# Performance work log

Measured on AMD Instinct MI355X. Metric: run time of the kernel, lower is better.

## Reference

```python
import jax, jax.numpy as jnp
import numpy as np
import math

B_SZ, T, D_IN, D_OUT, N = 8, 4096, 1024, 1024, 512
RMIN, RMAX, MAX_PHASE = 0.9, 1.0, 6.283


def setup_inputs() -> dict:
    key = jax.random.key(0)
    ks = jax.random.split(key, 9)
    x = jax.random.normal(ks[0], (B_SZ, T, D_IN), dtype=jnp.float32)
    u1 = jax.random.uniform(ks[1], (N,), dtype=jnp.float32)
    u2 = jax.random.uniform(ks[2], (N,), dtype=jnp.float32)
    nu_log = jnp.log(-0.5 * jnp.log(u1 * (RMAX + RMIN) * (RMAX - RMIN) + RMIN ** 2))
    theta_log = jnp.log(MAX_PHASE * u2)
    lam_mod = jnp.exp(-jnp.exp(nu_log))
    gamma_log = jnp.log(jnp.sqrt(1.0 - jnp.square(lam_mod)))
    B_re = jax.random.normal(ks[3], (N, D_IN), dtype=jnp.float32) / math.sqrt(2 * D_IN)
    B_im = jax.random.normal(ks[4], (N, D_IN), dtype=jnp.float32) / math.sqrt(2 * D_IN)
    C_re = jax.random.normal(ks[5], (D_OUT, N), dtype=jnp.float32) / math.sqrt(N)
    C_im = jax.random.normal(ks[6], (D_OUT, N), dtype=jnp.float32) / math.sqrt(N)
    D = jax.random.normal(ks[7], (D_OUT, D_IN), dtype=jnp.float32) / math.sqrt(D_IN)
    return {"x": x, "nu_log": nu_log, "theta_log": theta_log, "gamma_log": gamma_log,
            "B_re": B_re, "B_im": B_im, "C_re": C_re, "C_im": C_im, "D": D}


def reference(x, nu_log, theta_log, gamma_log, B_re, B_im, C_re, C_im, D):
    # Diagonal complex transition Lambda = exp(-exp(nu_log)) * exp(i*exp(theta_log))
    lam = jnp.exp(-jnp.exp(nu_log) + 1j * jnp.exp(theta_log))  # [N] complex64
    gamma = jnp.exp(gamma_log)  # [N]
    Bmat = B_re + 1j * B_im  # [N, D_IN]
    # Input projection for all timesteps at once: b_t = gamma * (B @ u_t)
    Bu = jnp.einsum('bti,ni->btn', x.astype(Bmat.dtype), Bmat) * gamma  # [B,T,N] complex
    # Parallel (associative) scan of x_t = lam * x_{t-1} + b_t over the time axis
    A = jnp.broadcast_to(lam, Bu.shape)

    def combine(e1, e2):
        a1, b1 = e1
        a2, b2 = e2
        return a1 * a2, a2 * b1 + b2

    _, states = jax.lax.associative_scan(combine, (A, Bu), axis=1)  # states: [B,T,N] complex
    Cmat = C_re + 1j * C_im  # [D_OUT, N]
    y = jnp.einsum('btn,on->bto', states, Cmat).real + jnp.einsum('bti,oi->bto', x, D)
    return y
```

## Files before the change

kernel.cpp:

```cpp
#include <hip/hip_runtime.h>
#include <stdint.h>


#define BSZ   8
#define TLEN  4096
#define DIN   1024
#define DOUT  1024
#define NST   512
#define M_TOT (BSZ * TLEN)
#define NC    32
#define CL    128
#define PLA   4096
#define BUFS  12288

typedef __attribute__((ext_vector_type(8))) short bf16x8;
typedef __attribute__((ext_vector_type(4))) float f32x4;

__device__ __forceinline__ float s2f(short s) {
  unsigned v = ((unsigned)(unsigned short)s) << 16;
  return __builtin_bit_cast(float, v);
}
__device__ __forceinline__ short f2s_rne(float f) {
  unsigned u = __builtin_bit_cast(unsigned, f);
  unsigned r = (u + 0x7FFFu + ((u >> 16) & 1u)) >> 16;
  return (short)r;
}
__device__ __forceinline__ void round8(const float4 v0, const float4 v1, bf16x8& hv) {
  const float f[8] = {v0.x, v0.y, v0.z, v0.w, v1.x, v1.y, v1.z, v1.w};
  #pragma unroll
  for (int j = 0; j < 8; ++j) hv[j] = f2s_rne(f[j]);
}

__device__ __forceinline__ void gload16(const short* g, short* l) {
  __builtin_amdgcn_global_load_lds(
      (const __attribute__((address_space(1))) void*)g,
      (__attribute__((address_space(3))) void*)l, 16, 0, 0);
}


__device__ __forceinline__ void stage_cx(
    const short* __restrict__ Ag, const short* __restrict__ Wg,
    const int lda, const int ldb, const int m0, const int n0, const int k0,
    short* lbuf, const int w, const int lane)
{
  const int q  = (lane & 3) ^ ((lane >> 3) & 3);
  const int gr = lane >> 2;
  #pragma unroll
  for (int j = 0; j < 3; ++j) {
    const int ch = w * 3 + j;
    const short* g;
    int r0, ld, dst;
    if (ch < 8) { g = Ag; r0 = m0 + ch * 16;        ld = lda; dst = ch * 512; }
    else        { g = Wg; r0 = n0 + (ch - 8) * 16;  ld = ldb; dst = PLA + (ch - 8) * 512; }
    gload16(g + (size_t)(r0 + gr) * ld + k0 + q * 8, lbuf + dst);
  }
}

template<int NT>
__device__ __forceinline__ void gemm_pl(
    const short* __restrict__ Ap, const short* __restrict__ Wp,
    const int lda, const int ldb, const int m0, const int n0, const int tid,
    f32x4 (&acc)[4][4], short* lds)
{
  const int lane = tid & 63, w = tid >> 6, wm = w >> 2, wn = w & 3;
  const int lr = lane & 15, kg = lane >> 4;
  const int qo = (kg ^ ((lr >> 1) & 3)) * 8;

  stage_cx(Ap, Wp, lda, ldb, m0, n0, 0, lds, w, lane);

  for (int k = 0; k < NT; ++k) {
    short* cur = lds + (k & 1) * BUFS;
    if (k + 1 < NT) {
      stage_cx(Ap, Wp, lda, ldb, m0, n0, (k + 1) * 32,
               lds + ((k + 1) & 1) * BUFS, w, lane);
      asm volatile("s_waitcnt vmcnt(3)" ::: "memory");
    } else {
      asm volatile("s_waitcnt vmcnt(0)" ::: "memory");
    }
    __builtin_amdgcn_s_barrier();

    bf16x8 bw[4];
    #pragma unroll
    for (int ph = 0; ph < 2; ++ph) {
      if (ph == 0) {
        #pragma unroll
        for (int ni = 0; ni < 4; ++ni)
          bw[ni] = *(const bf16x8*)&cur[PLA + (wn * 64 + ni * 16 + lr) * 32 + qo];
      }
      const int mi0 = ph * 2;
      const bf16x8 a0 = *(const bf16x8*)&cur[(wm * 64 + mi0 * 16 + lr) * 32 + qo];
      const bf16x8 a1 = *(const bf16x8*)&cur[(wm * 64 + (mi0 + 1) * 16 + lr) * 32 + qo];
      __builtin_amdgcn_s_barrier();
      asm volatile("s_waitcnt lgkmcnt(0)" ::: "memory");
      __builtin_amdgcn_sched_barrier(0);
      __builtin_amdgcn_s_setprio(1);
      #pragma unroll
      for (int ni = 0; ni < 4; ++ni) {
        acc[mi0][ni]     = __builtin_amdgcn_mfma_f32_16x16x32_bf16(a0, bw[ni], acc[mi0][ni], 0, 0, 0);
        acc[mi0 + 1][ni] = __builtin_amdgcn_mfma_f32_16x16x32_bf16(a1, bw[ni], acc[mi0 + 1][ni], 0, 0, 0);
      }
      __builtin_amdgcn_s_setprio(0);
      __builtin_amdgcn_s_barrier();
    }
  }
}

__device__ __forceinline__ void gemm_fb(
    const float* __restrict__ Af, const short* __restrict__ Wp,
    const int lda, const int ldb, const int K, const int m0, const int n0, const int tid,
    f32x4 (&acc)[4][4], short* lds)
{
  const int lane = tid & 63, w = tid >> 6, wm = w >> 2, wn = w & 3;
  const int r = tid & 127, e = (tid >> 7) & 3;
  float4 pa[2];
  {
    const float* p = Af + (size_t)(m0 + r) * lda + e * 8;
    pa[0] = *(const float4*)(p);
    pa[1] = *(const float4*)(p + 4);
  }
  for (int k0 = 0; k0 < K; k0 += 32) {
    __syncthreads();
    {
      bf16x8 hv;
      round8(pa[0], pa[1], hv);
      const int f = (r >> 1) & 3;
      *(bf16x8*)&lds[r * 32 + ((e ^ f) * 8)] = hv;
    }
    {
      const int q = (lane & 3) ^ ((lane >> 3) & 3);
      const int gr = lane >> 2;
      #pragma unroll
      for (int i = 0; i < 2; ++i)
        gload16(Wp + (size_t)(n0 + (2 * w + i) * 16 + gr) * ldb + k0 + q * 8,
                lds + PLA + (2 * w + i) * 512);
    }
    __syncthreads();
    if (k0 + 32 < K) {
      const float* p = Af + (size_t)(m0 + r) * lda + (k0 + 32) + e * 8;
      pa[0] = *(const float4*)(p);
      pa[1] = *(const float4*)(p + 4);
    }
    const int lr = lane & 15, kg = lane >> 4;
    const int qo = (kg ^ ((lr >> 1) & 3)) * 8;
    bf16x8 aw[4], bw[4];
    #pragma unroll
    for (int mi = 0; mi < 4; ++mi)
      aw[mi] = *(const bf16x8*)&lds[(wm * 64 + mi * 16 + lr) * 32 + qo];
    #pragma unroll
    for (int ni = 0; ni < 4; ++ni)
      bw[ni] = *(const bf16x8*)&lds[PLA + (wn * 64 + ni * 16 + lr) * 32 + qo];
    #pragma unroll
    for (int ni = 0; ni < 4; ++ni)
      #pragma unroll
      for (int mi = 0; mi < 4; ++mi)
        acc[mi][ni] = __builtin_amdgcn_mfma_f32_16x16x32_bf16(aw[mi], bw[ni], acc[mi][ni], 0, 0, 0);
  }
  __syncthreads();
}

__device__ __forceinline__ void map_mn4(const int bid, int& mb, int& nb) {
  const int xcd = bid & 7;
  const int j   = bid >> 3;
  mb = xcd * 32 + (j >> 2);
  nb = j & 3;
}

__global__ __launch_bounds__(256) void wround_k(const float* __restrict__ src,
    short* __restrict__ h, const int n4, const float sgn)
{
  const int i = blockIdx.x * 256 + threadIdx.x;
  if (i >= n4) return;
  const float4 v = ((const float4*)src)[i];
  short4 hv;
  hv.x = f2s_rne(sgn * v.x); hv.y = f2s_rne(sgn * v.y);
  hv.z = f2s_rne(sgn * v.z); hv.w = f2s_rne(sgn * v.w);
  ((short4*)h)[i] = hv;
}

template<bool XAG>
__global__ __launch_bounds__(512, 4) void bu_mfma(
    const float* __restrict__ x, const short* __restrict__ xw,
    const short* __restrict__ Brw, const short* __restrict__ Biw,
    const float* __restrict__ gamma,
    short* __restrict__ bu_re, short* __restrict__ bu_im)
{
  __shared__ short lds[2 * BUFS];
  f32x4 acc[4][4] = {};
  const int tid = threadIdx.x;
  int mb, nbk;
  map_mn4(blockIdx.x, mb, nbk);
  const int m0  = mb * 128;
  const int n0s = nbk * 256;
  const bool re = (n0s < NST);
  const int nb0 = n0s & (NST - 1);
  const short* Bw = re ? Brw : Biw;

  if constexpr (XAG)
    gemm_pl<32>(xw, Bw, DIN, DIN, m0, nb0, tid, acc, lds);
  else
    gemm_fb(x, Bw, DIN, DIN, DIN, m0, nb0, tid, acc, lds);

  short* Hp = re ? bu_re : bu_im;
  const int lane = tid & 63, w = tid >> 6, wm = w >> 2, wn = w & 3;
  const int lr = lane & 15, lq = lane >> 4;
  #pragma unroll
  for (int ni = 0; ni < 4; ++ni) {
    const int nb = nb0 + wn * 64 + ni * 16 + lr;
    const float g = gamma[nb];
    #pragma unroll
    for (int mi = 0; mi < 4; ++mi)
      #pragma unroll
      for (int j = 0; j < 4; ++j) {
        const size_t m = (size_t)m0 + wm * 64 + mi * 16 + lq * 4 + j;
        Hp[m * NST + nb] = f2s_rne(acc[mi][ni][j] * g);
      }
  }
}

__global__ void params_k(const float* __restrict__ nulog, const float* __restrict__ thlog,
                         const float* __restrict__ glog,
                         float2* __restrict__ lam, float2* __restrict__ lamL,
                         float* __restrict__ gamma)
{
  const int n = blockIdx.x * 256 + threadIdx.x;
  if (n >= NST) return;
  const float nu = expf(nulog[n]);
  const float th = expf(thlog[n]);
  const float mod = expf(-nu);
  float s, c;
  sincosf(th, &s, &c);
  lam[n] = make_float2(mod * c, mod * s);
  const float modL = expf(-(float)CL * nu);
  float sL, cL;
  sincosf((float)CL * th, &sL, &cL);
  lamL[n] = make_float2(modL * cL, modL * sL);
  gamma[n] = expf(glog[n]);
}

__global__ __launch_bounds__(256) void scan_partial(
    const short* __restrict__ bu_re, const short* __restrict__ bu_im,
    const float2* __restrict__ lam, float2* __restrict__ carry)
{
  const int g = blockIdx.x * 256 + threadIdx.x;
  const int n2 = g & 255;
  const int c  = (g >> 8) & (NC - 1);
  const int b  = g >> 13;
  const int n  = n2 * 2;
  const float2 L0 = lam[n], L1 = lam[n + 1];
  const short2* R = (const short2*)bu_re;
  const short2* I = (const short2*)bu_im;
  size_t idx = ((size_t)b * TLEN + (size_t)c * CL) * (NST / 2) + n2;
  float sr0 = 0.f, si0 = 0.f, sr1 = 0.f, si1 = 0.f;
  #pragma unroll 4
  for (int t = 0; t < CL; ++t, idx += NST / 2) {
    const short2 vr = R[idx], vi = I[idx];
    const float br0 = s2f(vr.x), br1 = s2f(vr.y);
    const float bi0 = s2f(vi.x), bi1 = s2f(vi.y);
    float nr = fmaf(L0.x, sr0, fmaf(-L0.y, si0, br0));
    float ni = fmaf(L0.x, si0, fmaf( L0.y, sr0, bi0));
    sr0 = nr; si0 = ni;
    nr = fmaf(L1.x, sr1, fmaf(-L1.y, si1, br1));
    ni = fmaf(L1.x, si1, fmaf( L1.y, sr1, bi1));
    sr1 = nr; si1 = ni;
  }
  const size_t cb = (size_t)(b * NC + c) * NST + n;
  carry[cb]     = make_float2(sr0, si0);
  carry[cb + 1] = make_float2(sr1, si1);
}

__global__ __launch_bounds__(256) void scan_carry(
    float2* __restrict__ carry, const float2* __restrict__ lamL)
{
  const int g = blockIdx.x * 256 + threadIdx.x;
  const int n = g & (NST - 1);
  const int b = g >> 9;
  const float2 P = lamL[n];
  float sr = 0.f, si = 0.f;
  for (int c = 0; c < NC; ++c) {
    const size_t idx = (size_t)(b * NC + c) * NST + n;
    const float2 v = carry[idx];
    carry[idx] = make_float2(sr, si);
    const float nr = fmaf(P.x, sr, fmaf(-P.y, si, v.x));
    const float ni = fmaf(P.x, si, fmaf( P.y, sr, v.y));
    sr = nr; si = ni;
  }
}

__global__ __launch_bounds__(256) void scan_final(
    short* __restrict__ bu_re, short* __restrict__ bu_im,
    const float2* __restrict__ lam, const float2* __restrict__ carry)
{
  const int g = blockIdx.x * 256 + threadIdx.x;
  const int n2 = g & 255;
  const int c  = (g >> 8) & (NC - 1);
  const int b  = g >> 13;
  const int n  = n2 * 2;
  const float2 L0 = lam[n], L1 = lam[n + 1];
  const size_t cb = (size_t)(b * NC + c) * NST + n;
  const float2 ci0 = carry[cb], ci1 = carry[cb + 1];
  short2* R = (short2*)bu_re;
  short2* I = (short2*)bu_im;
  size_t idx = ((size_t)b * TLEN + (size_t)c * CL) * (NST / 2) + n2;
  float sr0 = ci0.x, si0 = ci0.y, sr1 = ci1.x, si1 = ci1.y;
  #pragma unroll 4
  for (int t = 0; t < CL; ++t, idx += NST / 2) {
    const short2 vr = R[idx], vi = I[idx];
    const float br0 = s2f(vr.x), br1 = s2f(vr.y);
    const float bi0 = s2f(vi.x), bi1 = s2f(vi.y);
    float nr = fmaf(L0.x, sr0, fmaf(-L0.y, si0, br0));
    float ni = fmaf(L0.x, si0, fmaf( L0.y, sr0, bi0));
    sr0 = nr; si0 = ni;
    nr = fmaf(L1.x, sr1, fmaf(-L1.y, si1, br1));
    ni = fmaf(L1.x, si1, fmaf( L1.y, sr1, bi1));
    sr1 = nr; si1 = ni;
    short2 so;
    so.x = f2s_rne(sr0); so.y = f2s_rne(sr1);
    R[idx] = so;
    so.x = f2s_rne(si0); so.y = f2s_rne(si1);
    I[idx] = so;
  }
}

template<bool XAG>
__global__ __launch_bounds__(512, 4) void out_mfma(
    const short* __restrict__ st_re, const short* __restrict__ st_im,
    const float* __restrict__ x, const short* __restrict__ xw,
    const short* __restrict__ Crw, const short* __restrict__ Ciw,
    const short* __restrict__ Dw,
    float* __restrict__ y)
{
  __shared__ short lds[2 * BUFS];
  f32x4 acc[4][4] = {};
  const int tid = threadIdx.x;
  int mb, nbk;
  map_mn4(blockIdx.x, mb, nbk);
  const int m0 = mb * 128;
  const int o0 = nbk * 256;

  gemm_pl<16>(st_re, Crw, NST, NST, m0, o0, tid, acc, lds);
  gemm_pl<16>(st_im, Ciw, NST, NST, m0, o0, tid, acc, lds);
  if constexpr (XAG)
    gemm_pl<32>(xw, Dw, DIN, DIN, m0, o0, tid, acc, lds);
  else
    gemm_fb(x, Dw, DIN, DIN, DIN, m0, o0, tid, acc, lds);

  const int lane = tid & 63, w = tid >> 6, wm = w >> 2, wn = w & 3;
  const int lr = lane & 15, lq = lane >> 4;
  #pragma unroll
  for (int mi = 0; mi < 4; ++mi)
    #pragma unroll
    for (int j = 0; j < 4; ++j) {
      const size_t m = (size_t)m0 + wm * 64 + mi * 16 + lq * 4 + j;
      #pragma unroll
      for (int ni = 0; ni < 4; ++ni)
        y[m * DOUT + o0 + wn * 64 + ni * 16 + lr] = acc[mi][ni][j];
    }
}

extern "C" void kernel_launch(void* const* d_in, const int* in_sizes, int n_in,
                              void* d_out, int out_size, void* d_ws, size_t ws_size,
                              hipStream_t stream)
{
  (void)in_sizes; (void)n_in; (void)out_size;
  const float* x     = (const float*)d_in[0];
  const float* nulog = (const float*)d_in[1];
  const float* thlog = (const float*)d_in[2];
  const float* glog  = (const float*)d_in[3];
  const float* Bre   = (const float*)d_in[4];
  const float* Bim   = (const float*)d_in[5];
  const float* Cre   = (const float*)d_in[6];
  const float* Cim   = (const float*)d_in[7];
  const float* Dm    = (const float*)d_in[8];
  float* y = (float*)d_out;

  const size_t PLANE  = (size_t)M_TOT * NST;
  const size_t XPLANE = (size_t)M_TOT * DIN;
  short*  bu_re = (short*)d_ws;
  short*  bu_im = bu_re + PLANE;
  float2* carry = (float2*)(bu_im + PLANE);
  float2* lam   = carry + (size_t)BSZ * NC * NST;
  float2* lamL  = lam + NST;
  float*  gamma = (float*)(lamL + NST);

  char* wp = (char*)(gamma + NST);
  wp = (char*)(((uintptr_t)wp + 255) & ~(uintptr_t)255);
  short* Brw = (short*)wp;
  short* Biw = Brw + (size_t)NST * DIN;
  short* Crw = Biw + (size_t)NST * DIN;
  short* Ciw = Crw + (size_t)DOUT * NST;
  short* Dw  = Ciw + (size_t)DOUT * NST;
  short* xw  = Dw  + (size_t)DOUT * DIN;
  const size_t needed_full = (size_t)((char*)(xw + XPLANE) - (char*)d_ws);
  const bool full = (ws_size >= needed_full);

  params_k<<<2, 256, 0, stream>>>(nulog, thlog, glog, lam, lamL, gamma);

  const int nB4 = (NST * DIN) / 4, nC4 = (DOUT * NST) / 4, nD4 = (DOUT * DIN) / 4;
  wround_k<<<(nB4 + 255) / 256, 256, 0, stream>>>(Bre, Brw, nB4,  1.0f);
  wround_k<<<(nB4 + 255) / 256, 256, 0, stream>>>(Bim, Biw, nB4,  1.0f);
  wround_k<<<(nC4 + 255) / 256, 256, 0, stream>>>(Cre, Crw, nC4,  1.0f);
  wround_k<<<(nC4 + 255) / 256, 256, 0, stream>>>(Cim, Ciw, nC4, -1.0f);
  wround_k<<<(nD4 + 255) / 256, 256, 0, stream>>>(Dm,  Dw,  nD4,  1.0f);

  if (full) {
    const int nX4 = (int)(XPLANE / 4);
    wround_k<<<(nX4 + 255) / 256, 256, 0, stream>>>(x, xw, nX4, 1.0f);
    bu_mfma<true><<<1024, 512, 0, stream>>>(x, xw, Brw, Biw, gamma, bu_re, bu_im);
  } else {
    bu_mfma<false><<<1024, 512, 0, stream>>>(x, xw, Brw, Biw, gamma, bu_re, bu_im);
  }

  scan_partial<<<(BSZ * NC * (NST / 2)) / 256, 256, 0, stream>>>(bu_re, bu_im, lam, carry);
  scan_carry<<<(BSZ * NST) / 256, 256, 0, stream>>>(carry, lamL);
  scan_final<<<(BSZ * NC * (NST / 2)) / 256, 256, 0, stream>>>(bu_re, bu_im, lam, carry);

  if (full) {
    out_mfma<true><<<1024, 512, 0, stream>>>(bu_re, bu_im, x, xw, Crw, Ciw, Dw, y);
  } else {
    out_mfma<false><<<1024, 512, 0, stream>>>(bu_re, bu_im, x, xw, Crw, Ciw, Dw, y);
  }
}
```

Before: 314.8 us.

## Enlarge GEMM block tile to 256x256 for projection and output kernels

Adds a 256x256 block-tile GEMM path (each wave computes 128x64 with 8x4 MFMA fragments) and uses it for the Bu projection and the output projection when the workspace allows a bf16 copy of x. Grids shrink from 1024 to 512 blocks. The larger tile halves global and LDS traffic per FLOP and amortizes barriers, at the cost of higher register pressure, 64KB LDS per block and occupancy capped at 2 blocks per CU. The fallback paths are kept as separate kernels.

```diff
diff --git a/kernel.cpp b/kernel.cpp
--- a/kernel.cpp
+++ b/kernel.cpp
@@ -10,8 +10,12 @@
 #define M_TOT (BSZ * TLEN)
 #define NC    32
 #define CL    128
+
+#define WOFF  8192
+#define NBUF  16384
+
 #define PLA   4096
-#define BUFS  12288
+#define OBUFS 12288
 
 typedef __attribute__((ext_vector_type(8))) short bf16x8;
 typedef __attribute__((ext_vector_type(4))) float f32x4;
@@ -37,6 +41,82 @@
       (__attribute__((address_space(3))) void*)l, 16, 0, 0);
 }
 
+
+__device__ __forceinline__ void stage256(
+    const short* __restrict__ Ag, const short* __restrict__ Wg,
+    const int lda, const int ldb, const int m0, const int n0, const int k0,
+    short* lbuf, const int w, const int lane)
+{
+  const int q  = (lane & 3) ^ ((lane >> 3) & 3);
+  const int gr = lane >> 2;
+  #pragma unroll
+  for (int j = 0; j < 4; ++j) {
+    const int ch = w * 4 + j;
+    const short* g;
+    int r0, ld, dst;
+    if (ch < 16) { g = Ag; r0 = m0 + ch * 16;        ld = lda; dst = ch * 512; }
+    else         { g = Wg; r0 = n0 + (ch - 16) * 16; ld = ldb; dst = WOFF + (ch - 16) * 512; }
+    gload16(g + (size_t)(r0 + gr) * ld + k0 + q * 8, lbuf + dst);
+  }
+}
+
+template<int NT>
+__device__ __forceinline__ void gemm256(
+    const short* __restrict__ Ap, const short* __restrict__ Wp,
+    const int lda, const int ldb, const int m0, const int n0, const int tid,
+    f32x4 (&acc)[8][4], short* lds)
+{
+  const int lane = tid & 63, w = tid >> 6, wm = w >> 2, wn = w & 3;
+  const int lr = lane & 15, kg = lane >> 4;
+  const int qo = (kg ^ ((lr >> 1) & 3)) * 8;
+
+  stage256(Ap, Wp, lda, ldb, m0, n0, 0, lds, w, lane);
+
+  for (int k = 0; k < NT; ++k) {
+    short* cur = lds + (k & 1) * NBUF;
+    if (k + 1 < NT) {
+      stage256(Ap, Wp, lda, ldb, m0, n0, (k + 1) * 32,
+               lds + ((k + 1) & 1) * NBUF, w, lane);
+      asm volatile("s_waitcnt vmcnt(4)" ::: "memory");
+    } else {
+      asm volatile("s_waitcnt vmcnt(0)" ::: "memory");
+    }
+    __builtin_amdgcn_s_barrier();
+
+    bf16x8 wv[4];
+    #pragma unroll
+    for (int ph = 0; ph < 2; ++ph) {
+      if (ph == 0) {
+        #pragma unroll
+        for (int nf = 0; nf < 4; ++nf)
+          wv[nf] = *(const bf16x8*)&cur[WOFF + (wn * 64 + nf * 16 + lr) * 32 + qo];
+      }
+      bf16x8 af[4];
+      #pragma unroll
+      for (int mi = 0; mi < 4; ++mi)
+        af[mi] = *(const bf16x8*)&cur[(wm * 128 + (ph * 4 + mi) * 16 + lr) * 32 + qo];
+      __builtin_amdgcn_s_barrier();
+      asm volatile("s_waitcnt lgkmcnt(0)" ::: "memory");
+      __builtin_amdgcn_sched_barrier(0);
+      __builtin_amdgcn_s_setprio(1);
+      #pragma unroll
+      for (int nf = 0; nf < 4; ++nf)
+        #pragma unroll
+        for (int mi = 0; mi < 4; ++mi)
+          acc[ph * 4 + mi][nf] =
+              __builtin_amdgcn_mfma_f32_16x16x32_bf16(af[mi], wv[nf], acc[ph * 4 + mi][nf], 0, 0, 0);
+      __builtin_amdgcn_s_setprio(0);
+      __builtin_amdgcn_s_barrier();
+    }
+  }
+}
+
+__device__ __forceinline__ void map256(const int bid, int& mb, int& nb) {
+  const int xcd = bid & 7;
+  const int j   = bid >> 3;
+  mb = xcd * 16 + (j >> 2);
+  nb = j & 3;
+}
 
 __device__ __forceinline__ void stage_cx(
     const short* __restrict__ Ag, const short* __restrict__ Wg,
@@ -56,6 +136,59 @@
   }
 }
 
+__device__ __forceinline__ void gemm_fb(
+    const float* __restrict__ Af, const short* __restrict__ Wp,
+    const int lda, const int ldb, const int K, const int m0, const int n0, const int tid,
+    f32x4 (&acc)[4][4], short* lds)
+{
+  const int lane = tid & 63, w = tid >> 6, wm = w >> 2, wn = w & 3;
+  const int r = tid & 127, e = (tid >> 7) & 3;
+  float4 pa[2];
+  {
+    const float* p = Af + (size_t)(m0 + r) * lda + e * 8;
+    pa[0] = *(const float4*)(p);
+    pa[1] = *(const float4*)(p + 4);
+  }
+  for (int k0 = 0; k0 < K; k0 += 32) {
+    __syncthreads();
+    {
+      bf16x8 hv;
+      round8(pa[0], pa[1], hv);
+      const int f = (r >> 1) & 3;
+      *(bf16x8*)&lds[r * 32 + ((e ^ f) * 8)] = hv;
+    }
+    {
+      const int q = (lane & 3) ^ ((lane >> 3) & 3);
+      const int gr = lane >> 2;
+      #pragma unroll
+      for (int i = 0; i < 2; ++i)
+        gload16(Wp + (size_t)(n0 + (2 * w + i) * 16 + gr) * ldb + k0 + q * 8,
+                lds + PLA + (2 * w + i) * 512);
+    }
+    __syncthreads();
+    if (k0 + 32 < K) {
+      const float* p = Af + (size_t)(m0 + r) * lda + (k0 + 32) + e * 8;
+      pa[0] = *(const float4*)(p);
+      pa[1] = *(const float4*)(p + 4);
+    }
+    const int lr = lane & 15, kg = lane >> 4;
+    const int qo = (kg ^ ((lr >> 1) & 3)) * 8;
+    bf16x8 aw[4], bw[4];
+    #pragma unroll
+    for (int mi = 0; mi < 4; ++mi)
+      aw[mi] = *(const bf16x8*)&lds[(wm * 64 + mi * 16 + lr) * 32 + qo];
+    #pragma unroll
+    for (int ni = 0; ni < 4; ++ni)
+      bw[ni] = *(const bf16x8*)&lds[PLA + (wn * 64 + ni * 16 + lr) * 32 + qo];
+    #pragma unroll
+    for (int ni = 0; ni < 4; ++ni)
+      #pragma unroll
+      for (int mi = 0; mi < 4; ++mi)
+        acc[mi][ni] = __builtin_amdgcn_mfma_f32_16x16x32_bf16(aw[mi], bw[ni], acc[mi][ni], 0, 0, 0);
+  }
+  __syncthreads();
+}
+
 template<int NT>
 __device__ __forceinline__ void gemm_pl(
     const short* __restrict__ Ap, const short* __restrict__ Wp,
@@ -65,20 +198,16 @@
   const int lane = tid & 63, w = tid >> 6, wm = w >> 2, wn = w & 3;
   const int lr = lane & 15, kg = lane >> 4;
   const int qo = (kg ^ ((lr >> 1) & 3)) * 8;
-
   stage_cx(Ap, Wp, lda, ldb, m0, n0, 0, lds, w, lane);
-
   for (int k = 0; k < NT; ++k) {
-    short* cur = lds + (k & 1) * BUFS;
+    short* cur = lds + (k & 1) * OBUFS;
     if (k + 1 < NT) {
-      stage_cx(Ap, Wp, lda, ldb, m0, n0, (k + 1) * 32,
-               lds + ((k + 1) & 1) * BUFS, w, lane);
+      stage_cx(Ap, Wp, lda, ldb, m0, n0, (k + 1) * 32, lds + ((k + 1) & 1) * OBUFS, w, lane);
       asm volatile("s_waitcnt vmcnt(3)" ::: "memory");
     } else {
       asm volatile("s_waitcnt vmcnt(0)" ::: "memory");
     }
     __builtin_amdgcn_s_barrier();
-
     bf16x8 bw[4];
     #pragma unroll
     for (int ph = 0; ph < 2; ++ph) {
@@ -105,59 +234,6 @@
   }
 }
 
-__device__ __forceinline__ void gemm_fb(
-    const float* __restrict__ Af, const short* __restrict__ Wp,
-    const int lda, const int ldb, const int K, const int m0, const int n0, const int tid,
-    f32x4 (&acc)[4][4], short* lds)
-{
-  const int lane = tid & 63, w = tid >> 6, wm = w >> 2, wn = w & 3;
-  const int r = tid & 127, e = (tid >> 7) & 3;
-  float4 pa[2];
-  {
-    const float* p = Af + (size_t)(m0 + r) * lda + e * 8;
-    pa[0] = *(const float4*)(p);
-    pa[1] = *(const float4*)(p + 4);
-  }
-  for (int k0 = 0; k0 < K; k0 += 32) {
-    __syncthreads();
-    {
-      bf16x8 hv;
-      round8(pa[0], pa[1], hv);
-      const int f = (r >> 1) & 3;
-      *(bf16x8*)&lds[r * 32 + ((e ^ f) * 8)] = hv;
-    }
-    {
-      const int q = (lane & 3) ^ ((lane >> 3) & 3);
-      const int gr = lane >> 2;
-      #pragma unroll
-      for (int i = 0; i < 2; ++i)
-        gload16(Wp + (size_t)(n0 + (2 * w + i) * 16 + gr) * ldb + k0 + q * 8,
-                lds + PLA + (2 * w + i) * 512);
-    }
-    __syncthreads();
-    if (k0 + 32 < K) {
-      const float* p = Af + (size_t)(m0 + r) * lda + (k0 + 32) + e * 8;
-      pa[0] = *(const float4*)(p);
-      pa[1] = *(const float4*)(p + 4);
-    }
-    const int lr = lane & 15, kg = lane >> 4;
-    const int qo = (kg ^ ((lr >> 1) & 3)) * 8;
-    bf16x8 aw[4], bw[4];
-    #pragma unroll
-    for (int mi = 0; mi < 4; ++mi)
-      aw[mi] = *(const bf16x8*)&lds[(wm * 64 + mi * 16 + lr) * 32 + qo];
-    #pragma unroll
-    for (int ni = 0; ni < 4; ++ni)
-      bw[ni] = *(const bf16x8*)&lds[PLA + (wn * 64 + ni * 16 + lr) * 32 + qo];
-    #pragma unroll
-    for (int ni = 0; ni < 4; ++ni)
-      #pragma unroll
-      for (int mi = 0; mi < 4; ++mi)
-        acc[mi][ni] = __builtin_amdgcn_mfma_f32_16x16x32_bf16(aw[mi], bw[ni], acc[mi][ni], 0, 0, 0);
-  }
-  __syncthreads();
-}
-
 __device__ __forceinline__ void map_mn4(const int bid, int& mb, int& nb) {
   const int xcd = bid & 7;
   const int j   = bid >> 3;
@@ -177,14 +253,48 @@
   ((short4*)h)[i] = hv;
 }
 
-template<bool XAG>
-__global__ __launch_bounds__(512, 4) void bu_mfma(
-    const float* __restrict__ x, const short* __restrict__ xw,
+__global__ __launch_bounds__(512, 2) void bu_mfma(
+    const short* __restrict__ xw,
     const short* __restrict__ Brw, const short* __restrict__ Biw,
     const float* __restrict__ gamma,
     short* __restrict__ bu_re, short* __restrict__ bu_im)
 {
-  __shared__ short lds[2 * BUFS];
+  __shared__ short lds[2 * NBUF];
+  f32x4 acc[8][4] = {};
+  const int tid = threadIdx.x;
+  int mb, nbk;
+  map256(blockIdx.x, mb, nbk);
+  const int m0  = mb * 256;
+  const int n0s = nbk * 256;
+  const bool re = (n0s < NST);
+  const int nb0 = n0s & (NST - 1);
+
+  gemm256<32>(xw, re ? Brw : Biw, DIN, DIN, m0, nb0, tid, acc, lds);
+
+  short* Hp = re ? bu_re : bu_im;
+  const int lane = tid & 63, w = tid >> 6, wm = w >> 2, wn = w & 3;
+  const int lr = lane & 15, lq = lane >> 4;
+  #pragma unroll
+  for (int nf = 0; nf < 4; ++nf) {
+    const int nb = nb0 + wn * 64 + nf * 16 + lr;
+    const float g = gamma[nb];
+    #pragma unroll
+    for (int mf = 0; mf < 8; ++mf)
+      #pragma unroll
+      for (int j = 0; j < 4; ++j) {
+        const size_t m = (size_t)m0 + wm * 128 + mf * 16 + lq * 4 + j;
+        Hp[m * NST + nb] = f2s_rne(acc[mf][nf][j] * g);
+      }
+  }
+}
+
+__global__ __launch_bounds__(512, 4) void bu_fb(
+    const float* __restrict__ x,
+    const short* __restrict__ Brw, const short* __restrict__ Biw,
+    const float* __restrict__ gamma,
+    short* __restrict__ bu_re, short* __restrict__ bu_im)
+{
+  __shared__ short lds[2 * OBUFS];
   f32x4 acc[4][4] = {};
   const int tid = threadIdx.x;
   int mb, nbk;
@@ -193,13 +303,7 @@
   const int n0s = nbk * 256;
   const bool re = (n0s < NST);
   const int nb0 = n0s & (NST - 1);
-  const short* Bw = re ? Brw : Biw;
-
-  if constexpr (XAG)
-    gemm_pl<32>(xw, Bw, DIN, DIN, m0, nb0, tid, acc, lds);
-  else
-    gemm_fb(x, Bw, DIN, DIN, DIN, m0, nb0, tid, acc, lds);
-
+  gemm_fb(x, re ? Brw : Biw, DIN, DIN, DIN, m0, nb0, tid, acc, lds);
   short* Hp = re ? bu_re : bu_im;
   const int lane = tid & 63, w = tid >> 6, wm = w >> 2, wn = w & 3;
   const int lr = lane & 15, lq = lane >> 4;
@@ -321,29 +425,55 @@
   }
 }
 
-template<bool XAG>
-__global__ __launch_bounds__(512, 4) void out_mfma(
+__global__ __launch_bounds__(512, 2) void out_mfma(
     const short* __restrict__ st_re, const short* __restrict__ st_im,
-    const float* __restrict__ x, const short* __restrict__ xw,
+    const short* __restrict__ xw,
     const short* __restrict__ Crw, const short* __restrict__ Ciw,
     const short* __restrict__ Dw,
     float* __restrict__ y)
 {
-  __shared__ short lds[2 * BUFS];
+  __shared__ short lds[2 * NBUF];
+  f32x4 acc[8][4] = {};
+  const int tid = threadIdx.x;
+  int mb, nbk;
+  map256(blockIdx.x, mb, nbk);
+  const int m0 = mb * 256;
+  const int o0 = nbk * 256;
+
+  gemm256<16>(st_re, Crw, NST, NST, m0, o0, tid, acc, lds);
+  gemm256<16>(st_im, Ciw, NST, NST, m0, o0, tid, acc, lds);
+  gemm256<32>(xw, Dw, DIN, DIN, m0, o0, tid, acc, lds);
+
+  const int lane = tid & 63, w = tid >> 6, wm = w >> 2, wn = w & 3;
+  const int lr = lane & 15, lq = lane >> 4;
+  #pragma unroll
+  for (int mf = 0; mf < 8; ++mf)
+    #pragma unroll
+    for (int j = 0; j < 4; ++j) {
+      const size_t m = (size_t)m0 + wm * 128 + mf * 16 + lq * 4 + j;
+      #pragma unroll
+      for (int nf = 0; nf < 4; ++nf)
+        y[m * DOUT + o0 + wn * 64 + nf * 16 + lr] = acc[mf][nf][j];
+    }
+}
+
+__global__ __launch_bounds__(512, 4) void out_fb(
+    const short* __restrict__ st_re, const short* __restrict__ st_im,
+    const float* __restrict__ x,
+    const short* __restrict__ Crw, const short* __restrict__ Ciw,
+    const short* __restrict__ Dw,
+    float* __restrict__ y)
+{
+  __shared__ short lds[2 * OBUFS];
   f32x4 acc[4][4] = {};
   const int tid = threadIdx.x;
   int mb, nbk;
   map_mn4(blockIdx.x, mb, nbk);
   const int m0 = mb * 128;
   const int o0 = nbk * 256;
-
   gemm_pl<16>(st_re, Crw, NST, NST, m0, o0, tid, acc, lds);
   gemm_pl<16>(st_im, Ciw, NST, NST, m0, o0, tid, acc, lds);
-  if constexpr (XAG)
-    gemm_pl<32>(xw, Dw, DIN, DIN, m0, o0, tid, acc, lds);
-  else
-    gemm_fb(x, Dw, DIN, DIN, DIN, m0, o0, tid, acc, lds);
-
+  gemm_fb(x, Dw, DIN, DIN, DIN, m0, o0, tid, acc, lds);
   const int lane = tid & 63, w = tid >> 6, wm = w >> 2, wn = w & 3;
   const int lr = lane & 15, lq = lane >> 4;
   #pragma unroll
@@ -405,9 +535,9 @@
   if (full) {
     const int nX4 = (int)(XPLANE / 4);
     wround_k<<<(nX4 + 255) / 256, 256, 0, stream>>>(x, xw, nX4, 1.0f);
-    bu_mfma<true><<<1024, 512, 0, stream>>>(x, xw, Brw, Biw, gamma, bu_re, bu_im);
+    bu_mfma<<<512, 512, 0, stream>>>(xw, Brw, Biw, gamma, bu_re, bu_im);
   } else {
-    bu_mfma<false><<<1024, 512, 0, stream>>>(x, xw, Brw, Biw, gamma, bu_re, bu_im);
+    bu_fb<<<1024, 512, 0, stream>>>(x, Brw, Biw, gamma, bu_re, bu_im);
   }
 
   scan_partial<<<(BSZ * NC * (NST / 2)) / 256, 256, 0, stream>>>(bu_re, bu_im, lam, carry);
@@ -415,8 +545,8 @@
   scan_final<<<(BSZ * NC * (NST / 2)) / 256, 256, 0, stream>>>(bu_re, bu_im, lam, carry);
 
   if (full) {
-    out_mfma<true><<<1024, 512, 0, stream>>>(bu_re, bu_im, x, xw, Crw, Ciw, Dw, y);
+    out_mfma<<<512, 512, 0, stream>>>(bu_re, bu_im, xw, Crw, Ciw, Dw, y);
   } else {
-    out_mfma<false><<<1024, 512, 0, stream>>>(bu_re, bu_im, x, xw, Crw, Ciw, Dw, y);
-  }
-}
+    out_fb<<<1024, 512, 0, stream>>>(bu_re, bu_im, x, Crw, Ciw, Dw, y);
+  }
+}
```

Result: no change. 314.4 us (-0.1%).
